# Optimization experiments

Hardware: AMD Instinct MI355X
Metric: run time of the kernel (lower is better)

Reference implementation:

```python
import jax, jax.numpy as jnp
import numpy as np

# NTU RGB+D skeleton parent connectivity (from the original module's self.conn)
CONN = np.array([0, 0, 1, 2, 0, 4, 5, 3, 6, 9, 9, 12, 24, 11, 12,
                 13, 14, 15, 16, 15, 16, 15, 16, 11, 23], dtype=np.int32)


def setup_inputs() -> dict:
    key = jax.random.key(0)
    N, C, T, V, M = 128, 3, 300, 25, 2
    x = jax.random.normal(key, (N, C, T, V, M), dtype=jnp.float32)
    conn = jnp.asarray(CONN)
    return {"x": x, "conn": conn}


def reference(x, conn):
    # x: (N, C, T, V, M). Faithful vectorization of EfficientGCN.preprocess.
    N, C, T, V, M = x.shape
    eps = jnp.asarray(1e-4, x.dtype)

    # --- joint branch: [x ; x - x_center] where center joint index = 1 ---
    rel = x - x[:, :, :, 1:2, :]                      # (N,C,T,V,M)
    joint = jnp.concatenate([x, rel], axis=1)         # (N,2C,T,V,M)

    # --- velocity branch: 1-step and 2-step finite differences,
    #     filled for frames 0..T-3, last two frames are zero ---
    zeros2 = jnp.zeros((N, C, 2, V, M), dtype=x.dtype)
    v1 = jnp.concatenate([x[:, :, 1:T-1] - x[:, :, 0:T-2], zeros2], axis=2)
    v2 = jnp.concatenate([x[:, :, 2:T] - x[:, :, 0:T-2], zeros2], axis=2)
    velocity = jnp.concatenate([v1, v2], axis=1)      # (N,2C,T,V,M)

    # --- bone branch: joint - parent(joint), plus per-axis angle via acos ---
    bone_vec = x - x[:, :, :, conn, :]                # (N,C,T,V,M) gather along V
    bone_length = jnp.sqrt(jnp.sum(bone_vec * bone_vec, axis=1, keepdims=True)) + eps
    bone_ang = jnp.arccos(bone_vec / bone_length)     # (N,C,T,V,M)
    bone = jnp.concatenate([bone_vec, bone_ang], axis=1)  # (N,2C,T,V,M)

    # stack branches: (N, 3, 2C, T, V, M)
    return jnp.stack([joint, velocity, bone], axis=1)
```

## Files before the change

kernel.cpp:

```cpp
#include <hip/hip_runtime.h>
#include <math.h>


#define NN 128
#define CC 3
#define TT 300
#define VV 25
#define MM 2

typedef float f32x4 __attribute__((ext_vector_type(4)));
typedef float f32x2 __attribute__((ext_vector_type(2)));

constexpr int TVM  = TT * VV * MM;
constexpr int TV   = TT * VV;
constexpr int Q    = TV / 2;
constexpr int OUTP = 3 * 6 * TVM;

__global__ __launch_bounds__(256)
void egcn_pre_kernel(const float* __restrict__ x,
                     const int* __restrict__ conn,
                     float* __restrict__ out) {
    int j = blockIdx.x * blockDim.x + threadIdx.x;
    if (j >= NN * Q) return;

    int n   = j / Q;
    int k   = j - n * Q;
    int rv0 = 2 * k;
    int rv1 = rv0 + 1;
    int t0 = rv0 / VV, v0 = rv0 - t0 * VV;
    int t1 = rv1 / VV, v1 = rv1 - t1 * VV;

    int pa = conn[v0];
    int pb = conn[v1];
    bool hva = (t0 < TT - 2);
    bool hvb = (t1 < TT - 2);
    bool ld2 = (rv0 + 51 < TV);

    const float* xn = x + (size_t)n * CC * TVM;

    f32x4 xv[3], x2[3];
    f32x2 x1a[3], x1b[3], xca[3], xcb[3], xpa[3], xpb[3];
    #pragma unroll
    for (int c = 0; c < 3; ++c) {
        const float*  pc = xn + c * TVM;
        const f32x2* p2 = reinterpret_cast<const f32x2*>(pc);
        const f32x4* p4 = reinterpret_cast<const f32x4*>(pc);
        xv[c]  = p4[k];
        x2[c]  = ld2 ? p4[k + VV] : (f32x4)(0.f);
        x1a[c] = hva ? p2[rv0 + VV] : (f32x2)(0.f);
        x1b[c] = hvb ? p2[rv1 + VV] : (f32x2)(0.f);
        xca[c] = p2[t0 * VV + 1];
        xcb[c] = p2[t1 * VV + 1];
        xpa[c] = p2[t0 * VV + pa];
        xpb[c] = p2[t1 * VV + pb];
    }

    f32x2 bva[3], bvb[3];
    float sa0 = 0.f, sa1 = 0.f, sb0 = 0.f, sb1 = 0.f;
    #pragma unroll
    for (int c = 0; c < 3; ++c) {
        bva[c].x = xv[c].x - xpa[c].x;
        bva[c].y = xv[c].y - xpa[c].y;
        bvb[c].x = xv[c].z - xpb[c].x;
        bvb[c].y = xv[c].w - xpb[c].y;
        sa0 += bva[c].x * bva[c].x;  sa1 += bva[c].y * bva[c].y;
        sb0 += bvb[c].x * bvb[c].x;  sb1 += bvb[c].y * bvb[c].y;
    }
    float ia0 = 1.0f / (sqrtf(sa0) + 1e-4f);
    float ia1 = 1.0f / (sqrtf(sa1) + 1e-4f);
    float ib0 = 1.0f / (sqrtf(sb0) + 1e-4f);
    float ib1 = 1.0f / (sqrtf(sb1) + 1e-4f);

    f32x4* o4 = reinterpret_cast<f32x4*>(out + (size_t)n * OUTP);
    #pragma unroll
    for (int c = 0; c < 3; ++c) {
        __builtin_nontemporal_store(xv[c], &o4[(0 * 6 + c) * Q + k]);
        f32x4 rel;
        rel.x = xv[c].x - xca[c].x;  rel.y = xv[c].y - xca[c].y;
        rel.z = xv[c].z - xcb[c].x;  rel.w = xv[c].w - xcb[c].y;
        __builtin_nontemporal_store(rel, &o4[(0 * 6 + c + 3) * Q + k]);

        f32x4 u1, u2;
        u1.x = hva ? x1a[c].x - xv[c].x : 0.f;
        u1.y = hva ? x1a[c].y - xv[c].y : 0.f;
        u1.z = hvb ? x1b[c].x - xv[c].z : 0.f;
        u1.w = hvb ? x1b[c].y - xv[c].w : 0.f;
        u2.x = hva ? x2[c].x - xv[c].x : 0.f;
        u2.y = hva ? x2[c].y - xv[c].y : 0.f;
        u2.z = hvb ? x2[c].z - xv[c].z : 0.f;
        u2.w = hvb ? x2[c].w - xv[c].w : 0.f;
        __builtin_nontemporal_store(u1, &o4[(1 * 6 + c) * Q + k]);
        __builtin_nontemporal_store(u2, &o4[(1 * 6 + c + 3) * Q + k]);

        f32x4 bn, ang;
        bn.x = bva[c].x;  bn.y = bva[c].y;  bn.z = bvb[c].x;  bn.w = bvb[c].y;
        __builtin_nontemporal_store(bn, &o4[(2 * 6 + c) * Q + k]);
        ang.x = acosf(bva[c].x * ia0);
        ang.y = acosf(bva[c].y * ia1);
        ang.z = acosf(bvb[c].x * ib0);
        ang.w = acosf(bvb[c].y * ib1);
        __builtin_nontemporal_store(ang, &o4[(2 * 6 + c + 3) * Q + k]);
    }
}

extern "C" void kernel_launch(void* const* d_in, const int* in_sizes, int n_in,
                              void* d_out, int out_size, void* d_ws, size_t ws_size,
                              hipStream_t stream) {
    const float* x   = (const float*)d_in[0];
    const int* conn  = (const int*)d_in[1];
    float* out       = (float*)d_out;

    int total = NN * Q;
    int block = 256;
    int grid  = (total + block - 1) / block;
    egcn_pre_kernel<<<grid, block, 0, stream>>>(x, conn, out);
}
```

Before: 164.7 us.

## Stage per-sample 20-frame tiles with halo in LDS before computing outputs

```diff
diff --git a/kernel.cpp b/kernel.cpp
--- a/kernel.cpp
+++ b/kernel.cpp
@@ -11,48 +11,70 @@
 typedef float f32x4 __attribute__((ext_vector_type(4)));
 typedef float f32x2 __attribute__((ext_vector_type(2)));
 
-constexpr int TVM  = TT * VV * MM;
-constexpr int TV   = TT * VV;
-constexpr int Q    = TV / 2;
-constexpr int OUTP = 3 * 6 * TVM;
+constexpr int TVM   = TT * VV * MM;
+constexpr int TV    = TT * VV;
+constexpr int Q     = TV / 2;
+constexpr int OUTP  = 3 * 6 * TVM;
+
+constexpr int TBF    = 20;
+constexpr int HALO   = 2;
+constexpr int CHUNKS = TT / TBF;
+constexpr int F4PB   = TBF * VV / 2;
+constexpr int FRF    = VV * MM;
+constexpr int LDS_FL = (TBF + HALO) * FRF;
 
 __global__ __launch_bounds__(256)
 void egcn_pre_kernel(const float* __restrict__ x,
                      const int* __restrict__ conn,
                      float* __restrict__ out) {
-    int j = blockIdx.x * blockDim.x + threadIdx.x;
-    if (j >= NN * Q) return;
+    __shared__ float lds[3 * LDS_FL];
+    __shared__ int   connS[VV];
 
-    int n   = j / Q;
-    int k   = j - n * Q;
-    int rv0 = 2 * k;
-    int rv1 = rv0 + 1;
-    int t0 = rv0 / VV, v0 = rv0 - t0 * VV;
-    int t1 = rv1 / VV, v1 = rv1 - t1 * VV;
+    int bid = blockIdx.x;
+    int n   = bid / CHUNKS;
+    int blk = bid - n * CHUNKS;
+    int tid = threadIdx.x;
 
-    int pa = conn[v0];
-    int pb = conn[v1];
-    bool hva = (t0 < TT - 2);
-    bool hvb = (t1 < TT - 2);
-    bool ld2 = (rv0 + 51 < TV);
+    int t0     = blk * TBF;
+    int frames = min(TBF + HALO, TT - t0);
+    int nf4    = frames * FRF / 4;
 
     const float* xn = x + (size_t)n * CC * TVM;
+
+    if (tid < VV) connS[tid] = conn[tid];
+    #pragma unroll
+    for (int c = 0; c < 3; ++c) {
+        const f32x4* p4 = reinterpret_cast<const f32x4*>(xn + c * TVM + t0 * FRF);
+        f32x4* l4 = reinterpret_cast<f32x4*>(lds + c * LDS_FL);
+        for (int i = tid; i < nf4; i += 256) l4[i] = p4[i];
+    }
+    __syncthreads();
+
+    if (tid >= F4PB) return;
+
+    int sa  = 2 * tid;
+    int sb  = sa + 1;
+    int tla = sa / VV, va = sa - tla * VV;
+    int tlb = sb / VV, vb = sb - tlb * VV;
+    int pa  = connS[va];
+    int pb  = connS[vb];
+    bool hva = (t0 + tla) < TT - 2;
+    bool hvb = (t0 + tlb) < TT - 2;
 
     f32x4 xv[3], x2[3];
     f32x2 x1a[3], x1b[3], xca[3], xcb[3], xpa[3], xpb[3];
     #pragma unroll
     for (int c = 0; c < 3; ++c) {
-        const float*  pc = xn + c * TVM;
-        const f32x2* p2 = reinterpret_cast<const f32x2*>(pc);
-        const f32x4* p4 = reinterpret_cast<const f32x4*>(pc);
-        xv[c]  = p4[k];
-        x2[c]  = ld2 ? p4[k + VV] : (f32x4)(0.f);
-        x1a[c] = hva ? p2[rv0 + VV] : (f32x2)(0.f);
-        x1b[c] = hvb ? p2[rv1 + VV] : (f32x2)(0.f);
-        xca[c] = p2[t0 * VV + 1];
-        xcb[c] = p2[t1 * VV + 1];
-        xpa[c] = p2[t0 * VV + pa];
-        xpb[c] = p2[t1 * VV + pb];
+        const float* lc = lds + c * LDS_FL;
+        const f32x2* L2 = reinterpret_cast<const f32x2*>(lc);
+        xv[c]  = *reinterpret_cast<const f32x4*>(lc + 4 * tid);
+        x2[c]  = *reinterpret_cast<const f32x4*>(lc + 4 * tid + 2 * FRF);
+        x1a[c] = L2[sa + VV];
+        x1b[c] = L2[sb + VV];
+        xca[c] = L2[tla * VV + 1];
+        xcb[c] = L2[tlb * VV + 1];
+        xpa[c] = L2[tla * VV + pa];
+        xpb[c] = L2[tlb * VV + pb];
     }
 
     f32x2 bva[3], bvb[3];
@@ -71,6 +93,7 @@
     float ib0 = 1.0f / (sqrtf(sb0) + 1e-4f);
     float ib1 = 1.0f / (sqrtf(sb1) + 1e-4f);
 
+    int k = blk * F4PB + tid;
     f32x4* o4 = reinterpret_cast<f32x4*>(out + (size_t)n * OUTP);
     #pragma unroll
     for (int c = 0; c < 3; ++c) {
@@ -110,8 +133,6 @@
     const int* conn  = (const int*)d_in[1];
     float* out       = (float*)d_out;
 
-    int total = NN * Q;
-    int block = 256;
-    int grid  = (total + block - 1) / block;
-    egcn_pre_kernel<<<grid, block, 0, stream>>>(x, conn, out);
+    int grid = NN * CHUNKS;
+    egcn_pre_kernel<<<grid, 256, 0, stream>>>(x, conn, out);
 }
```

New measurement: 166.2 us. Within noise of the previous version (+0.9%).
